# Kernel tuning notes

Hardware: AMD Instinct MI355X
Metric: run time of the kernel (lower is better)

Reference implementation:

```python
import jax, jax.numpy as jnp
import numpy as np

E = 16
TOP_K = 2


def setup_inputs() -> dict:
    key = jax.random.key(0)
    k1, k2, k3, k4, k5 = jax.random.split(key, 5)
    H, I = 2048, 1408
    scale = 0.02  # typical init scale, keeps activations numerically tame
    return {
        "hidden_states": jax.random.normal(k1, (4, 2048, H), dtype=jnp.float32),
        "gate_w": jax.random.normal(k2, (H, E), dtype=jnp.float32) * scale,
        "w1": jax.random.normal(k3, (E, H, I), dtype=jnp.float32) * scale,
        "w3": jax.random.normal(k4, (E, H, I), dtype=jnp.float32) * scale,
        "w2": jax.random.normal(k5, (E, I, H), dtype=jnp.float32) * scale,
    }


def reference(hidden_states, gate_w, w1, w3, w2):
    orig_shape = hidden_states.shape
    H = orig_shape[-1]
    x = hidden_states.reshape(-1, H)          # [T, H]
    T = x.shape[0]

    # Router: gate linear -> softmax -> top-k -> renormalize (norm_expert_weight=True)
    router_logits = x @ gate_w                # [T, E]
    probs = jax.nn.softmax(router_logits, axis=-1)
    topk_w, topk_i = jax.lax.top_k(probs, TOP_K)          # [T, K]
    topk_w = topk_w / jnp.sum(topk_w, axis=-1, keepdims=True)

    # Dense combine weights [T, E] (zero for non-selected experts)
    combine = jnp.zeros((T, E), dtype=x.dtype)
    combine = combine.at[jnp.arange(T)[:, None], topk_i].add(topk_w)

    # Grouped SwiGLU experts: out = sum_e combine[:, e] * ((silu(x@w1_e) * (x@w3_e)) @ w2_e)
    out = jnp.zeros_like(x)
    for e in range(E):  # fixed small expert count
        gate_act = jax.nn.silu(x @ w1[e])     # [T, I]
        up = x @ w3[e]                        # [T, I]
        y = (gate_act * up) @ w2[e]           # [T, H]
        out = out + combine[:, e:e + 1] * y

    return out.reshape(orig_shape)
```

## Files before the change

### kernel.cpp

```cpp
#include <hip/hip_runtime.h>
#include <hip/hip_bf16.h>

#define E_ 16
#define H_ 2048
#define I_ 1408
#define BM 128
#define BN 128
#define BK 32
#define SB 48

typedef __attribute__((ext_vector_type(8))) short bf16x8;
typedef __attribute__((ext_vector_type(4))) float f32x4;

__device__ __forceinline__ int swz(int row, int e) {
  return row * SB + ((((e >> 3) + (row >> 2)) & 3) << 3) + (e & 7);
}

__device__ __forceinline__ unsigned int pk2(float a, float b) {
  __hip_bfloat162 h = __float22bfloat162_rn(make_float2(a, b));
  unsigned int u;
  __builtin_memcpy(&u, &h, 4);
  return u;
}

__device__ __forceinline__ unsigned short bf16b(float a) {
  unsigned int u = __builtin_bit_cast(unsigned int, a);
  u = (u + 0x7fffu + ((u >> 16) & 1u)) >> 16;
  return (unsigned short)u;
}

__global__ __launch_bounds__(64) void moe_router(
    const float* __restrict__ x, const float* __restrict__ gw,
    int* __restrict__ counts, int* __restrict__ list2s,
    float* __restrict__ listw, int T)
{
  const int lane = threadIdx.x;
  const int t0 = blockIdx.x * 4;
  double acc[4][16];
#pragma unroll
  for (int i = 0; i < 4; ++i)
#pragma unroll
    for (int j = 0; j < 16; ++j) acc[i][j] = 0.0;

  const float4* gw4 = (const float4*)gw;
  for (int it = 0; it < H_ / 64; ++it) {
    const int h = it * 64 + lane;
    float gv[16];
    *(float4*)&gv[0]  = gw4[h * 4 + 0];
    *(float4*)&gv[4]  = gw4[h * 4 + 1];
    *(float4*)&gv[8]  = gw4[h * 4 + 2];
    *(float4*)&gv[12] = gw4[h * 4 + 3];
    float xr[4];
#pragma unroll
    for (int i = 0; i < 4; ++i) xr[i] = x[(size_t)(t0 + i) * H_ + h];
#pragma unroll
    for (int i = 0; i < 4; ++i) {
      const double xv = (double)xr[i];
#pragma unroll
      for (int j = 0; j < 16; ++j) acc[i][j] += xv * (double)gv[j];
    }
  }
#pragma unroll
  for (int i = 0; i < 4; ++i)
#pragma unroll
    for (int j = 0; j < 16; ++j) {
      double v = acc[i][j];
#pragma unroll
      for (int m = 32; m > 0; m >>= 1) v += __shfl_xor(v, m, 64);
      acc[i][j] = v;
    }
  if (lane == 0) {
#pragma unroll
    for (int i = 0; i < 4; ++i) {
      const int t = t0 + i;
      double b1 = -1e300, b2 = -1e300;
      int i1 = 0, i2 = 0;
#pragma unroll
      for (int j = 0; j < 16; ++j) {
        const double l = acc[i][j];
        if (l > b1) { b2 = b1; i2 = i1; b1 = l; i1 = j; }
        else if (l > b2) { b2 = l; i2 = j; }
      }
      const float ex = expf((float)(b2 - b1));
      const float wa = 1.f / (1.f + ex);
      const float wb = ex / (1.f + ex);
      int p = atomicAdd(&counts[i1], 1);
      list2s[i1 * T + p] = t * 2;
      listw[i1 * T + p] = wa;
      p = atomicAdd(&counts[i2], 1);
      list2s[i2 * T + p] = t * 2 + 1;
      listw[i2 * T + p] = wb;
    }
  }
}

__device__ __forceinline__ void stage_b(const float* __restrict__ bp,
                                        unsigned short* Bs, int bn, int bk, int ldb) {
  const float4 r0 = *(const float4*)(bp);
  const float4 r1 = *(const float4*)(bp + ldb);
  const float4 r2 = *(const float4*)(bp + 2 * ldb);
  const float4 r3 = *(const float4*)(bp + 3 * ldb);
  uint2 c;
  c.x = pk2(r0.x, r1.x); c.y = pk2(r2.x, r3.x);
  *(uint2*)&Bs[swz(bn + 0, bk)] = c;
  c.x = pk2(r0.y, r1.y); c.y = pk2(r2.y, r3.y);
  *(uint2*)&Bs[swz(bn + 1, bk)] = c;
  c.x = pk2(r0.z, r1.z); c.y = pk2(r2.z, r3.z);
  *(uint2*)&Bs[swz(bn + 2, bk)] = c;
  c.x = pk2(r0.w, r1.w); c.y = pk2(r2.w, r3.w);
  *(uint2*)&Bs[swz(bn + 3, bk)] = c;
}

__global__ __launch_bounds__(256) void moe_gemm1(
    const float* __restrict__ x, const float* __restrict__ w1,
    const float* __restrict__ w3, const int* __restrict__ counts,
    const int* __restrict__ list2s, unsigned short* __restrict__ act, int T)
{
  const int e = blockIdx.z;
  const int cnt = counts[e];
  const int m0 = blockIdx.y * BM;
  if (m0 >= cnt) return;
  const int n0 = blockIdx.x * BN;
  const float* w1e = w1 + (size_t)e * H_ * I_;
  const float* w3e = w3 + (size_t)e * H_ * I_;
  const int* lst = list2s + (size_t)e * T;

  __shared__ unsigned short As[BM * SB], B1s[BN * SB], B3s[BN * SB];

  const int tid = threadIdx.x;
  const int lane = tid & 63, wave = tid >> 6;
  const int wr = (wave >> 1) * 64, wc = (wave & 1) * 64;
  const int l16 = lane & 15, quad = lane >> 4;

  const int ar = tid >> 1, ahalf = tid & 1;
  const int apos = m0 + ar;
  const int a_t2s = lst[apos < cnt ? apos : cnt - 1];
  const float* aptr = x + (size_t)(a_t2s >> 1) * H_ + ahalf * 16;

  const int nq = tid & 31, kb = tid >> 5;
  const int bn = nq * 4, bk = kb * 4;

  f32x4 acc1[4][4], acc3[4][4];
  const f32x4 fz = {0.f, 0.f, 0.f, 0.f};
#pragma unroll
  for (int mi = 0; mi < 4; ++mi)
#pragma unroll
    for (int ni = 0; ni < 4; ++ni) { acc1[mi][ni] = fz; acc3[mi][ni] = fz; }

  for (int k0 = 0; k0 < H_; k0 += BK) {
    __syncthreads();
    {
      const float4 a0 = *(const float4*)(aptr + k0);
      const float4 a1 = *(const float4*)(aptr + k0 + 4);
      const float4 a2 = *(const float4*)(aptr + k0 + 8);
      const float4 a3 = *(const float4*)(aptr + k0 + 12);
      uint4 A0, A1;
      A0.x = pk2(a0.x, a0.y); A0.y = pk2(a0.z, a0.w);
      A0.z = pk2(a1.x, a1.y); A0.w = pk2(a1.z, a1.w);
      A1.x = pk2(a2.x, a2.y); A1.y = pk2(a2.z, a2.w);
      A1.z = pk2(a3.x, a3.y); A1.w = pk2(a3.z, a3.w);
      *(uint4*)&As[swz(ar, ahalf * 16)] = A0;
      *(uint4*)&As[swz(ar, ahalf * 16 + 8)] = A1;
    }
    stage_b(w1e + (size_t)(k0 + bk) * I_ + n0 + bn, B1s, bn, bk, I_);
    stage_b(w3e + (size_t)(k0 + bk) * I_ + n0 + bn, B3s, bn, bk, I_);
    __syncthreads();

    bf16x8 af[4], b1f[4], b3f[4];
#pragma unroll
    for (int mi = 0; mi < 4; ++mi)
      af[mi] = *(const bf16x8*)&As[swz(wr + mi * 16 + l16, quad * 8)];
#pragma unroll
    for (int ni = 0; ni < 4; ++ni) {
      b1f[ni] = *(const bf16x8*)&B1s[swz(wc + ni * 16 + l16, quad * 8)];
      b3f[ni] = *(const bf16x8*)&B3s[swz(wc + ni * 16 + l16, quad * 8)];
    }
#pragma unroll
    for (int mi = 0; mi < 4; ++mi)
#pragma unroll
      for (int ni = 0; ni < 4; ++ni) {
        acc1[mi][ni] = __builtin_amdgcn_mfma_f32_16x16x32_bf16(af[mi], b1f[ni], acc1[mi][ni], 0, 0, 0);
        acc3[mi][ni] = __builtin_amdgcn_mfma_f32_16x16x32_bf16(af[mi], b3f[ni], acc3[mi][ni], 0, 0, 0);
      }
  }

#pragma unroll
  for (int mi = 0; mi < 4; ++mi) {
    const int rbase = m0 + wr + mi * 16 + quad * 4;
#pragma unroll
    for (int r = 0; r < 4; ++r) {
      const int pos = rbase + r;
      if (pos < cnt) {
        const int t2s = lst[pos];
        unsigned short* op = act + (size_t)t2s * I_ + n0 + wc + l16;
#pragma unroll
        for (int ni = 0; ni < 4; ++ni) {
          const float g = acc1[mi][ni][r];
          const float u = acc3[mi][ni][r];
          const float s = g / (1.f + __expf(-g));
          op[ni * 16] = bf16b(s * u);
        }
      }
    }
  }
}

__global__ __launch_bounds__(256) void moe_gemm2(
    const unsigned short* __restrict__ act, const float* __restrict__ w2,
    const int* __restrict__ counts, const int* __restrict__ list2s,
    const float* __restrict__ listw, float* __restrict__ out, int T)
{
  const int e = blockIdx.z;
  const int cnt = counts[e];
  const int m0 = blockIdx.y * BM;
  if (m0 >= cnt) return;
  const int n0 = blockIdx.x * BN;
  const float* w2e = w2 + (size_t)e * I_ * H_;
  const int* lst = list2s + (size_t)e * T;
  const float* lw = listw + (size_t)e * T;

  __shared__ unsigned short As[BM * SB], Bs[BN * SB];

  const int tid = threadIdx.x;
  const int lane = tid & 63, wave = tid >> 6;
  const int wr = (wave >> 1) * 64, wc = (wave & 1) * 64;
  const int l16 = lane & 15, quad = lane >> 4;

  const int ar = tid >> 1, ahalf = tid & 1;
  const int apos = m0 + ar;
  const int a_t2s = lst[apos < cnt ? apos : cnt - 1];
  const unsigned short* aptr = act + (size_t)a_t2s * I_ + ahalf * 16;

  const int nq = tid & 31, kb = tid >> 5;
  const int bn = nq * 4, bk = kb * 4;

  f32x4 acc[4][4];
  const f32x4 fz = {0.f, 0.f, 0.f, 0.f};
#pragma unroll
  for (int mi = 0; mi < 4; ++mi)
#pragma unroll
    for (int ni = 0; ni < 4; ++ni) acc[mi][ni] = fz;

  for (int k0 = 0; k0 < I_; k0 += BK) {
    __syncthreads();
    {
      const uint4 A0 = *(const uint4*)(aptr + k0);
      const uint4 A1 = *(const uint4*)(aptr + k0 + 8);
      *(uint4*)&As[swz(ar, ahalf * 16)] = A0;
      *(uint4*)&As[swz(ar, ahalf * 16 + 8)] = A1;
    }
    stage_b(w2e + (size_t)(k0 + bk) * H_ + n0 + bn, Bs, bn, bk, H_);
    __syncthreads();

    bf16x8 af[4], bf[4];
#pragma unroll
    for (int mi = 0; mi < 4; ++mi)
      af[mi] = *(const bf16x8*)&As[swz(wr + mi * 16 + l16, quad * 8)];
#pragma unroll
    for (int ni = 0; ni < 4; ++ni)
      bf[ni] = *(const bf16x8*)&Bs[swz(wc + ni * 16 + l16, quad * 8)];
#pragma unroll
    for (int mi = 0; mi < 4; ++mi)
#pragma unroll
      for (int ni = 0; ni < 4; ++ni)
        acc[mi][ni] = __builtin_amdgcn_mfma_f32_16x16x32_bf16(af[mi], bf[ni], acc[mi][ni], 0, 0, 0);
  }

#pragma unroll
  for (int mi = 0; mi < 4; ++mi) {
    const int rbase = m0 + wr + mi * 16 + quad * 4;
#pragma unroll
    for (int r = 0; r < 4; ++r) {
      const int pos = rbase + r;
      if (pos < cnt) {
        const int t2s = lst[pos];
        const float wt = lw[pos];
        float* op = out + (size_t)(t2s >> 1) * H_ + n0 + wc + l16;
#pragma unroll
        for (int ni = 0; ni < 4; ++ni)
          atomicAdd(op + ni * 16, wt * acc[mi][ni][r]);
      }
    }
  }
}

extern "C" void kernel_launch(void* const* d_in, const int* in_sizes, int n_in,
                              void* d_out, int out_size, void* d_ws, size_t ws_size,
                              hipStream_t stream) {
  const float* x  = (const float*)d_in[0];
  const float* gw = (const float*)d_in[1];
  const float* w1 = (const float*)d_in[2];
  const float* w3 = (const float*)d_in[3];
  const float* w2 = (const float*)d_in[4];
  float* out = (float*)d_out;
  const int T = in_sizes[0] / H_;

  char* ws = (char*)d_ws;
  int* counts = (int*)ws;
  int* list2s = (int*)(ws + 256);
  float* listw = (float*)(ws + 256 + (size_t)E_ * T * 4);
  unsigned short* act = (unsigned short*)(ws + 256 + 2 * (size_t)E_ * T * 4);

  hipMemsetAsync(counts, 0, 256, stream);
  hipMemsetAsync(out, 0, (size_t)out_size * sizeof(float), stream);
  moe_router<<<T / 4, 64, 0, stream>>>(x, gw, counts, list2s, listw, T);
  moe_gemm1<<<dim3(I_ / BN, T / BM, E_), 256, 0, stream>>>(x, w1, w3, counts, list2s, act, T);
  moe_gemm2<<<dim3(H_ / BN, T / BM, E_), 256, 0, stream>>>(act, w2, counts, list2s, listw, out, T);
}
```

Before: 1.699 ms.

## Pre-convert activations and weights to transposed bf16 before grouped expert GEMMs

Adds conversion kernels that turn x into bf16 and each expert weight matrix into a transposed bf16 copy in workspace. The GEMM kernels then load contiguous bf16 K-slices straight into shared memory, removing the per-tile fp32-to-bf16 packing and the strided four-row gathers of B in the inner loop. The conversions run on every call, so all weights are read once in fp32 and written again as bf16 (roughly 1.1 GB of traffic), and the path needs a large workspace, falling back to the fp32 kernels otherwise.

```diff
diff --git a/kernel.cpp b/kernel.cpp
--- a/kernel.cpp
+++ b/kernel.cpp
@@ -90,6 +90,220 @@
       p = atomicAdd(&counts[i2], 1);
       list2s[i2 * T + p] = t * 2 + 1;
       listw[i2 * T + p] = wb;
+    }
+  }
+}
+
+__global__ __launch_bounds__(256) void convert_x(
+    const float* __restrict__ x, unsigned short* __restrict__ xb)
+{
+  const size_t idx = ((size_t)blockIdx.x * 256 + threadIdx.x) * 8;
+  const float4 f0 = *(const float4*)(x + idx);
+  const float4 f1 = *(const float4*)(x + idx + 4);
+  uint4 o;
+  o.x = pk2(f0.x, f0.y); o.y = pk2(f0.z, f0.w);
+  o.z = pk2(f1.x, f1.y); o.w = pk2(f1.z, f1.w);
+  *(uint4*)(xb + idx) = o;
+}
+
+__global__ __launch_bounds__(256) void convert_wT(
+    const float* __restrict__ src, unsigned short* __restrict__ dst,
+    int R, int C)
+{
+  const int e = blockIdx.z;
+  src += (size_t)e * R * C;
+  dst += (size_t)e * C * R;
+  const int r0 = blockIdx.y * 128 + (threadIdx.x >> 4) * 8;
+  const int c0 = blockIdx.x * 128 + (threadIdx.x & 15) * 8;
+  float av[8][8];
+#pragma unroll
+  for (int j = 0; j < 8; ++j) {
+    const float4 t0 = *(const float4*)(src + (size_t)(r0 + j) * C + c0);
+    const float4 t1 = *(const float4*)(src + (size_t)(r0 + j) * C + c0 + 4);
+    av[j][0] = t0.x; av[j][1] = t0.y; av[j][2] = t0.z; av[j][3] = t0.w;
+    av[j][4] = t1.x; av[j][5] = t1.y; av[j][6] = t1.z; av[j][7] = t1.w;
+  }
+#pragma unroll
+  for (int n = 0; n < 8; ++n) {
+    uint4 o;
+    o.x = pk2(av[0][n], av[1][n]);
+    o.y = pk2(av[2][n], av[3][n]);
+    o.z = pk2(av[4][n], av[5][n]);
+    o.w = pk2(av[6][n], av[7][n]);
+    *(uint4*)(dst + (size_t)(c0 + n) * R + r0) = o;
+  }
+}
+
+__global__ __launch_bounds__(256) void moe_gemm1_b16(
+    const unsigned short* __restrict__ xb, const unsigned short* __restrict__ w1b,
+    const unsigned short* __restrict__ w3b, const int* __restrict__ counts,
+    const int* __restrict__ list2s, unsigned short* __restrict__ act, int T)
+{
+  const int e = blockIdx.z;
+  const int cnt = counts[e];
+  const int m0 = blockIdx.y * BM;
+  if (m0 >= cnt) return;
+  const int n0 = blockIdx.x * BN;
+  const unsigned short* w1e = w1b + (size_t)e * H_ * I_;
+  const unsigned short* w3e = w3b + (size_t)e * H_ * I_;
+  const int* lst = list2s + (size_t)e * T;
+
+  __shared__ unsigned short As[BM * SB], B1s[BN * SB], B3s[BN * SB];
+
+  const int tid = threadIdx.x;
+  const int lane = tid & 63, wave = tid >> 6;
+  const int wr = (wave >> 1) * 64, wc = (wave & 1) * 64;
+  const int l16 = lane & 15, quad = lane >> 4;
+
+  const int ar = tid >> 1, ahalf = tid & 1;
+  const int apos = m0 + ar;
+  const int a_t2s = lst[apos < cnt ? apos : cnt - 1];
+  const unsigned short* aptr = xb + (size_t)(a_t2s >> 1) * H_ + ahalf * 16;
+  const unsigned short* b1p = w1e + (size_t)(n0 + ar) * H_ + ahalf * 16;
+  const unsigned short* b3p = w3e + (size_t)(n0 + ar) * H_ + ahalf * 16;
+
+  f32x4 acc1[4][4], acc3[4][4];
+  const f32x4 fz = {0.f, 0.f, 0.f, 0.f};
+#pragma unroll
+  for (int mi = 0; mi < 4; ++mi)
+#pragma unroll
+    for (int ni = 0; ni < 4; ++ni) { acc1[mi][ni] = fz; acc3[mi][ni] = fz; }
+
+  uint4 pA0, pA1, pB10, pB11, pB30, pB31;
+  pA0  = *(const uint4*)(aptr);     pA1  = *(const uint4*)(aptr + 8);
+  pB10 = *(const uint4*)(b1p);      pB11 = *(const uint4*)(b1p + 8);
+  pB30 = *(const uint4*)(b3p);      pB31 = *(const uint4*)(b3p + 8);
+
+  for (int k0 = 0; k0 < H_; k0 += BK) {
+    __syncthreads();
+    *(uint4*)&As[swz(ar, ahalf * 16)]      = pA0;
+    *(uint4*)&As[swz(ar, ahalf * 16 + 8)]  = pA1;
+    *(uint4*)&B1s[swz(ar, ahalf * 16)]     = pB10;
+    *(uint4*)&B1s[swz(ar, ahalf * 16 + 8)] = pB11;
+    *(uint4*)&B3s[swz(ar, ahalf * 16)]     = pB30;
+    *(uint4*)&B3s[swz(ar, ahalf * 16 + 8)] = pB31;
+    const int kn = (k0 + BK < H_) ? k0 + BK : 0;
+    pA0  = *(const uint4*)(aptr + kn);     pA1  = *(const uint4*)(aptr + kn + 8);
+    pB10 = *(const uint4*)(b1p + kn);      pB11 = *(const uint4*)(b1p + kn + 8);
+    pB30 = *(const uint4*)(b3p + kn);      pB31 = *(const uint4*)(b3p + kn + 8);
+    __syncthreads();
+
+    bf16x8 af[4], b1f[4], b3f[4];
+#pragma unroll
+    for (int mi = 0; mi < 4; ++mi)
+      af[mi] = *(const bf16x8*)&As[swz(wr + mi * 16 + l16, quad * 8)];
+#pragma unroll
+    for (int ni = 0; ni < 4; ++ni) {
+      b1f[ni] = *(const bf16x8*)&B1s[swz(wc + ni * 16 + l16, quad * 8)];
+      b3f[ni] = *(const bf16x8*)&B3s[swz(wc + ni * 16 + l16, quad * 8)];
+    }
+#pragma unroll
+    for (int mi = 0; mi < 4; ++mi)
+#pragma unroll
+      for (int ni = 0; ni < 4; ++ni) {
+        acc1[mi][ni] = __builtin_amdgcn_mfma_f32_16x16x32_bf16(af[mi], b1f[ni], acc1[mi][ni], 0, 0, 0);
+        acc3[mi][ni] = __builtin_amdgcn_mfma_f32_16x16x32_bf16(af[mi], b3f[ni], acc3[mi][ni], 0, 0, 0);
+      }
+  }
+
+#pragma unroll
+  for (int mi = 0; mi < 4; ++mi) {
+    const int rbase = m0 + wr + mi * 16 + quad * 4;
+#pragma unroll
+    for (int r = 0; r < 4; ++r) {
+      const int pos = rbase + r;
+      if (pos < cnt) {
+        const int t2s = lst[pos];
+        unsigned short* op = act + (size_t)t2s * I_ + n0 + wc + l16;
+#pragma unroll
+        for (int ni = 0; ni < 4; ++ni) {
+          const float g = acc1[mi][ni][r];
+          const float u = acc3[mi][ni][r];
+          const float s = g / (1.f + __expf(-g));
+          op[ni * 16] = bf16b(s * u);
+        }
+      }
+    }
+  }
+}
+
+__global__ __launch_bounds__(256) void moe_gemm2_b16(
+    const unsigned short* __restrict__ act, const unsigned short* __restrict__ w2b,
+    const int* __restrict__ counts, const int* __restrict__ list2s,
+    const float* __restrict__ listw, float* __restrict__ out, int T)
+{
+  const int e = blockIdx.z;
+  const int cnt = counts[e];
+  const int m0 = blockIdx.y * BM;
+  if (m0 >= cnt) return;
+  const int n0 = blockIdx.x * BN;
+  const unsigned short* w2e = w2b + (size_t)e * I_ * H_;
+  const int* lst = list2s + (size_t)e * T;
+  const float* lw = listw + (size_t)e * T;
+
+  __shared__ unsigned short As[BM * SB], Bs[BN * SB];
+
+  const int tid = threadIdx.x;
+  const int lane = tid & 63, wave = tid >> 6;
+  const int wr = (wave >> 1) * 64, wc = (wave & 1) * 64;
+  const int l16 = lane & 15, quad = lane >> 4;
+
+  const int ar = tid >> 1, ahalf = tid & 1;
+  const int apos = m0 + ar;
+  const int a_t2s = lst[apos < cnt ? apos : cnt - 1];
+  const unsigned short* aptr = act + (size_t)a_t2s * I_ + ahalf * 16;
+  const unsigned short* bp = w2e + (size_t)(n0 + ar) * I_ + ahalf * 16;
+
+  f32x4 acc[4][4];
+  const f32x4 fz = {0.f, 0.f, 0.f, 0.f};
+#pragma unroll
+  for (int mi = 0; mi < 4; ++mi)
+#pragma unroll
+    for (int ni = 0; ni < 4; ++ni) acc[mi][ni] = fz;
+
+  uint4 pA0, pA1, pB0, pB1;
+  pA0 = *(const uint4*)(aptr);  pA1 = *(const uint4*)(aptr + 8);
+  pB0 = *(const uint4*)(bp);    pB1 = *(const uint4*)(bp + 8);
+
+  for (int k0 = 0; k0 < I_; k0 += BK) {
+    __syncthreads();
+    *(uint4*)&As[swz(ar, ahalf * 16)]     = pA0;
+    *(uint4*)&As[swz(ar, ahalf * 16 + 8)] = pA1;
+    *(uint4*)&Bs[swz(ar, ahalf * 16)]     = pB0;
+    *(uint4*)&Bs[swz(ar, ahalf * 16 + 8)] = pB1;
+    const int kn = (k0 + BK < I_) ? k0 + BK : 0;
+    pA0 = *(const uint4*)(aptr + kn);  pA1 = *(const uint4*)(aptr + kn + 8);
+    pB0 = *(const uint4*)(bp + kn);    pB1 = *(const uint4*)(bp + kn + 8);
+    __syncthreads();
+
+    bf16x8 af[4], bf[4];
+#pragma unroll
+    for (int mi = 0; mi < 4; ++mi)
+      af[mi] = *(const bf16x8*)&As[swz(wr + mi * 16 + l16, quad * 8)];
+#pragma unroll
+    for (int ni = 0; ni < 4; ++ni)
+      bf[ni] = *(const bf16x8*)&Bs[swz(wc + ni * 16 + l16, quad * 8)];
+#pragma unroll
+    for (int mi = 0; mi < 4; ++mi)
+#pragma unroll
+      for (int ni = 0; ni < 4; ++ni)
+        acc[mi][ni] = __builtin_amdgcn_mfma_f32_16x16x32_bf16(af[mi], bf[ni], acc[mi][ni], 0, 0, 0);
+  }
+
+#pragma unroll
+  for (int mi = 0; mi < 4; ++mi) {
+    const int rbase = m0 + wr + mi * 16 + quad * 4;
+#pragma unroll
+    for (int r = 0; r < 4; ++r) {
+      const int pos = rbase + r;
+      if (pos < cnt) {
+        const int t2s = lst[pos];
+        const float wt = lw[pos];
+        float* op = out + (size_t)(t2s >> 1) * H_ + n0 + wc + l16;
+#pragma unroll
+        for (int ni = 0; ni < 4; ++ni)
+          atomicAdd(op + ni * 16, wt * acc[mi][ni][r]);
+      }
     }
   }
 }
@@ -111,7 +325,7 @@
   *(uint2*)&Bs[swz(bn + 3, bk)] = c;
 }
 
-__global__ __launch_bounds__(256) void moe_gemm1(
+__global__ __launch_bounds__(256) void moe_gemm1_f32(
     const float* __restrict__ x, const float* __restrict__ w1,
     const float* __restrict__ w3, const int* __restrict__ counts,
     const int* __restrict__ list2s, unsigned short* __restrict__ act, int T)
@@ -205,7 +419,7 @@
   }
 }
 
-__global__ __launch_bounds__(256) void moe_gemm2(
+__global__ __launch_bounds__(256) void moe_gemm2_f32(
     const unsigned short* __restrict__ act, const float* __restrict__ w2,
     const int* __restrict__ counts, const int* __restrict__ list2s,
     const float* __restrict__ listw, float* __restrict__ out, int T)
@@ -299,11 +513,32 @@
   int* counts = (int*)ws;
   int* list2s = (int*)(ws + 256);
   float* listw = (float*)(ws + 256 + (size_t)E_ * T * 4);
-  unsigned short* act = (unsigned short*)(ws + 256 + 2 * (size_t)E_ * T * 4);
+  const size_t o_act = 256 + 2 * (size_t)E_ * T * 4;
+  unsigned short* act = (unsigned short*)(ws + o_act);
+  const size_t o_xb  = o_act + 2 * (size_t)T * I_ * 2;
+  const size_t whi   = (size_t)E_ * H_ * I_ * 2;
+  const size_t o_w1b = o_xb + (size_t)T * H_ * 2;
+  const size_t o_w3b = o_w1b + whi;
+  const size_t o_w2b = o_w3b + whi;
+  const size_t need  = o_w2b + whi;
 
   hipMemsetAsync(counts, 0, 256, stream);
   hipMemsetAsync(out, 0, (size_t)out_size * sizeof(float), stream);
   moe_router<<<T / 4, 64, 0, stream>>>(x, gw, counts, list2s, listw, T);
-  moe_gemm1<<<dim3(I_ / BN, T / BM, E_), 256, 0, stream>>>(x, w1, w3, counts, list2s, act, T);
-  moe_gemm2<<<dim3(H_ / BN, T / BM, E_), 256, 0, stream>>>(act, w2, counts, list2s, listw, out, T);
-}
+
+  if (ws_size >= need) {
+    unsigned short* xb  = (unsigned short*)(ws + o_xb);
+    unsigned short* w1b = (unsigned short*)(ws + o_w1b);
+    unsigned short* w3b = (unsigned short*)(ws + o_w3b);
+    unsigned short* w2b = (unsigned short*)(ws + o_w2b);
+    convert_x<<<(size_t)T * H_ / 2048, 256, 0, stream>>>(x, xb);
+    convert_wT<<<dim3(I_ / 128, H_ / 128, E_), 256, 0, stream>>>(w1, w1b, H_, I_);
+    convert_wT<<<dim3(I_ / 128, H_ / 128, E_), 256, 0, stream>>>(w3, w3b, H_, I_);
+    convert_wT<<<dim3(H_ / 128, I_ / 128, E_), 256, 0, stream>>>(w2, w2b, I_, H_);
+    moe_gemm1_b16<<<dim3(I_ / BN, T / BM, E_), 256, 0, stream>>>(xb, w1b, w3b, counts, list2s, act, T);
+    moe_gemm2_b16<<<dim3(H_ / BN, T / BM, E_), 256, 0, stream>>>(act, w2b, counts, list2s, listw, out, T);
+  } else {
+    moe_gemm1_f32<<<dim3(I_ / BN, T / BM, E_), 256, 0, stream>>>(x, w1, w3, counts, list2s, act, T);
+    moe_gemm2_f32<<<dim3(H_ / BN, T / BM, E_), 256, 0, stream>>>(act, w2, counts, list2s, listw, out, T);
+  }
+}
```

Result: faster. 1.452 ms (-14.5%).
